# Performance work log

Hardware: AMD Instinct MI355X
Metric: run time of the kernel (lower is better)

Reference implementation:

```python
import jax, jax.numpy as jnp
import numpy as np

E, K, D_IN, D_OUT, D_HID = 16, 2, 1024, 1024, 2048

def setup_inputs() -> dict:
    key = jax.random.key(0)
    ks = jax.random.split(key, 6)
    s_in = 1.0 / np.sqrt(D_IN)
    s_hid = 1.0 / np.sqrt(D_HID)
    return {
        "x": jax.random.normal(ks[0], (4096, D_IN), dtype=jnp.float32),
        "gate_w": jax.random.uniform(ks[1], (E, D_IN), jnp.float32, -s_in, s_in),
        "w1": jax.random.uniform(ks[2], (E, D_HID, D_IN), jnp.float32, -s_in, s_in),
        "b1": jax.random.uniform(ks[3], (E, D_HID), jnp.float32, -s_in, s_in),
        "w2": jax.random.uniform(ks[4], (E, D_OUT, D_HID), jnp.float32, -s_hid, s_hid),
        "b2": jax.random.uniform(ks[5], (E, D_OUT), jnp.float32, -s_hid, s_hid),
    }

def reference(x, gate_w, w1, b1, w2, b2):
    # gate: [B, E]
    gate_scores = jnp.einsum('bi,ei->be', x, gate_w)
    topk_vals, topk_idxs = jax.lax.top_k(gate_scores, K)  # [B, K]
    topk_weights = jax.nn.softmax(topk_vals, axis=-1)     # [B, K]
    # dense all-expert MLP (faithful to reference): [B, E, D_OUT]
    h = jax.nn.relu(jnp.einsum('bi,ehi->beh', x, w1) + b1[None])
    expert_outputs = jnp.einsum('beh,eoh->beo', h, w2) + b2[None]
    # gather selected experts: [B, K, D_OUT]
    sel = jnp.take_along_axis(expert_outputs, topk_idxs[:, :, None], axis=1)
    return jnp.sum(sel * topk_weights[:, :, None], axis=1)
```

## Files before the change

kernel.cpp:

```cpp
#include <hip/hip_runtime.h>
#include <hip/hip_bf16.h>
#include <math.h>

#define B_TOK 4096
#define NE 16
#define DI 1024
#define DH 2048
#define DOUT 1024
#define NSLOT (B_TOK * 2)

typedef unsigned short u16;
typedef short bfrag __attribute__((ext_vector_type(8)));
typedef float f32x4 __attribute__((ext_vector_type(4)));
typedef u16 u16x8 __attribute__((ext_vector_type(8)));

__device__ __forceinline__ u16 f2bf(float f) {
    union { float f; unsigned u; } v; v.f = f;
    return (u16)((v.u + 0x7fffu + ((v.u >> 16) & 1u)) >> 16);
}

__device__ __forceinline__ void async16(const void* g, void* lds) {
    __builtin_amdgcn_global_load_lds(
        (const __attribute__((address_space(1))) void*)g,
        (__attribute__((address_space(3))) void*)lds,
        16, 0, 0);
}

__global__ void zero_init(float* __restrict__ out, int n4) {
    int i = blockIdx.x * blockDim.x + threadIdx.x;
    if (i < n4) ((float4*)out)[i] = make_float4(0.f, 0.f, 0.f, 0.f);
}

__global__ void convert_bf16(const float* __restrict__ src, u16* __restrict__ dst, int n8) {
    int i = blockIdx.x * blockDim.x + threadIdx.x;
    if (i >= n8) return;
    const float4* s4 = (const float4*)src;
    float4 a = s4[2 * i], b = s4[2 * i + 1];
    u16x8 r;
    r[0] = f2bf(a.x); r[1] = f2bf(a.y); r[2] = f2bf(a.z); r[3] = f2bf(a.w);
    r[4] = f2bf(b.x); r[5] = f2bf(b.y); r[6] = f2bf(b.z); r[7] = f2bf(b.w);
    ((u16x8*)dst)[i] = r;
}

__global__ __launch_bounds__(256) void gate_topk(
    const float* __restrict__ x, const float* __restrict__ gw,
    int* __restrict__ token_e, float* __restrict__ token_w)
{
    int wave = threadIdx.x >> 6, lane = threadIdx.x & 63;
    int t = blockIdx.x * 4 + wave;
    const float4* x4 = (const float4*)(x + (size_t)t * DI);
    const float4* g4 = (const float4*)gw;
    double acc[NE];
#pragma unroll
    for (int e = 0; e < NE; ++e) acc[e] = 0.0;
#pragma unroll
    for (int i = 0; i < 4; ++i) {
        float4 xv = x4[lane + i * 64];
#pragma unroll
        for (int e = 0; e < NE; ++e) {
            float4 gv = g4[e * 256 + lane + i * 64];
            acc[e] += (double)xv.x * gv.x + (double)xv.y * gv.y
                    + (double)xv.z * gv.z + (double)xv.w * gv.w;
        }
    }
#pragma unroll
    for (int e = 0; e < NE; ++e) {
        double v = acc[e];
        for (int off = 32; off; off >>= 1) v += __shfl_xor(v, off, 64);
        acc[e] = v;
    }
    if (lane == 0) {
        int e0 = 0; double v0 = acc[0];
#pragma unroll
        for (int e = 1; e < NE; ++e) if (acc[e] > v0) { v0 = acc[e]; e0 = e; }
        int e1 = -1; double v1 = -1e300;
#pragma unroll
        for (int e = 0; e < NE; ++e) if (e != e0 && acc[e] > v1) { v1 = acc[e]; e1 = e; }
        float d = expf((float)(v1 - v0));
        float w0 = 1.f / (1.f + d);
        float w1 = d * w0;
        token_e[2 * t] = e0; token_e[2 * t + 1] = e1;
        token_w[2 * t] = w0; token_w[2 * t + 1] = w1;
    }
}

__global__ __launch_bounds__(1024) void route(
    const int* __restrict__ token_e, const float* __restrict__ token_w,
    int* __restrict__ counts, int* __restrict__ offsets,
    int* __restrict__ slot_token, float* __restrict__ slot_wgt)
{
    __shared__ int lcnt[NE];
    __shared__ int lcur[NE];
    int tid = threadIdx.x;
    if (tid < NE) lcnt[tid] = 0;
    __syncthreads();
    for (int i = tid; i < NSLOT; i += 1024) atomicAdd(&lcnt[token_e[i]], 1);
    __syncthreads();
    if (tid == 0) {
        int s = 0;
        for (int e = 0; e < NE; ++e) {
            int c = lcnt[e];
            counts[e] = c; offsets[e] = s; lcur[e] = s; s += c;
        }
    }
    __syncthreads();
    for (int i = tid; i < NSLOT; i += 1024) {
        int e = token_e[i];
        int pos = atomicAdd(&lcur[e], 1);
        slot_token[pos] = i >> 1;
        slot_wgt[pos] = token_w[i];
    }
}

template <int PHASE>
__global__ __launch_bounds__(256) void moe_gemm(
    const u16* __restrict__ Abuf,
    const u16* __restrict__ Bbuf,
    const float* __restrict__ bias,
    const int* __restrict__ counts, const int* __restrict__ offsets,
    const int* __restrict__ slot_token, const float* __restrict__ slot_wgt,
    u16* __restrict__ hb, float* __restrict__ out)
{
    constexpr int KDIM = (PHASE == 1) ? DI : DH;
    constexpr int NDIM = (PHASE == 1) ? DH : DOUT;
    constexpr int NT = NDIM / 128;
    constexpr int MT = B_TOK / 128;
    constexpr int PER_XCD = (NE * NT * MT) / 8;

    const int id = blockIdx.x;
    const int wg = (id & 7) * PER_XCD + (id >> 3);
    const int e  = wg / (NT * MT);
    const int rem = wg % (NT * MT);
    const int nt = rem / MT;
    const int mt = rem % MT;

    const int cnt = counts[e];
    const int m0 = mt * 128;
    if (m0 >= cnt) return;
    const int n0 = nt * 128;
    const int sbase = offsets[e];

    __shared__ u16 ldsbuf[2][8192];

    const int tid = threadIdx.x;
    const int wv = tid >> 6, lane = tid & 63;
    const int lrow = lane >> 2, lkc = lane & 3;

    const int arow0 = wv * 16 + lrow;
    const int arow1 = 64 + wv * 16 + lrow;

    const u16* aptr0; const u16* aptr1;
    if (PHASE == 1) {
        int c = cnt - 1;
        int r0 = m0 + arow0; if (r0 > c) r0 = c;
        int r1 = m0 + arow1; if (r1 > c) r1 = c;
        aptr0 = Abuf + (size_t)slot_token[sbase + r0] * KDIM + lkc * 8;
        aptr1 = Abuf + (size_t)slot_token[sbase + r1] * KDIM + lkc * 8;
    } else {
        int s0 = sbase + m0 + arow0; if (s0 > NSLOT - 1) s0 = NSLOT - 1;
        int s1 = sbase + m0 + arow1; if (s1 > NSLOT - 1) s1 = NSLOT - 1;
        aptr0 = Abuf + (size_t)s0 * KDIM + lkc * 8;
        aptr1 = Abuf + (size_t)s1 * KDIM + lkc * 8;
    }
    const u16* bbase = Bbuf + (size_t)e * NDIM * KDIM;
    const u16* bptr0 = bbase + (size_t)(n0 + arow0) * KDIM + lkc * 8;
    const u16* bptr1 = bbase + (size_t)(n0 + arow1) * KDIM + lkc * 8;

    f32x4 acc[4][4];
#pragma unroll
    for (int i = 0; i < 4; ++i)
#pragma unroll
        for (int j = 0; j < 4; ++j) acc[i][j] = (f32x4){0.f, 0.f, 0.f, 0.f};

    const int wm = (wv & 1) * 64, wn = (wv >> 1) * 64;
    const int quad = lane >> 4, mr = lane & 15;
    const int aoff = (wm + mr) * 32 + quad * 8;
    const int boff = (wn + mr) * 32 + quad * 8;

    const int nk = KDIM / 32;

    {
        u16* base = &ldsbuf[0][0];
        async16(aptr0, base + wv * 512);
        async16(aptr1, base + 2048 + wv * 512);
        async16(bptr0, base + 4096 + wv * 512);
        async16(bptr1, base + 4096 + 2048 + wv * 512);
    }
    __syncthreads();

    for (int kt = 0; kt < nk; ++kt) {
        const int cur = kt & 1;
        if (kt + 1 < nk) {
            u16* base = &ldsbuf[cur ^ 1][0];
            const int ko = (kt + 1) * 32;
            async16(aptr0 + ko, base + wv * 512);
            async16(aptr1 + ko, base + 2048 + wv * 512);
            async16(bptr0 + ko, base + 4096 + wv * 512);
            async16(bptr1 + ko, base + 4096 + 2048 + wv * 512);
        }
        const u16* alds = &ldsbuf[cur][0];
        const u16* blds = alds + 4096;
        bfrag af[4], bf[4];
#pragma unroll
        for (int i = 0; i < 4; ++i) af[i] = *(const bfrag*)(alds + aoff + i * 512);
#pragma unroll
        for (int j = 0; j < 4; ++j) bf[j] = *(const bfrag*)(blds + boff + j * 512);
#pragma unroll
        for (int i = 0; i < 4; ++i)
#pragma unroll
            for (int j = 0; j < 4; ++j)
                acc[i][j] = __builtin_amdgcn_mfma_f32_16x16x32_bf16(af[i], bf[j], acc[i][j], 0, 0, 0);
        __syncthreads();
    }

    const float* bias_e = bias + e * NDIM;
    if constexpr (PHASE == 1) {
#pragma unroll
        for (int i = 0; i < 4; ++i) {
            int mbase = wm + i * 16 + quad * 4;
#pragma unroll
            for (int j = 0; j < 4; ++j) {
                int n = n0 + wn + j * 16 + mr;
                float bv = bias_e[n];
#pragma unroll
                for (int r = 0; r < 4; ++r) {
                    int m = m0 + mbase + r;
                    if (m < cnt) {
                        float v = acc[i][j][r] + bv;
                        v = v > 0.f ? v : 0.f;
                        hb[(size_t)(sbase + m) * DH + n] = f2bf(v);
                    }
                }
            }
        }
    } else {
#pragma unroll
        for (int i = 0; i < 4; ++i) {
            int mbase = wm + i * 16 + quad * 4;
#pragma unroll
            for (int r = 0; r < 4; ++r) {
                int m = m0 + mbase + r;
                if (m < cnt) {
                    int slot = sbase + m;
                    int tok = slot_token[slot];
                    float wgt = slot_wgt[slot];
                    float* orow = out + (size_t)tok * DOUT + n0 + wn;
#pragma unroll
                    for (int j = 0; j < 4; ++j) {
                        int nl = j * 16 + mr;
                        float v = wgt * (acc[i][j][r] + bias_e[n0 + wn + nl]);
                        atomicAdd(orow + nl, v);
                    }
                }
            }
        }
    }
}

extern "C" void kernel_launch(void* const* d_in, const int* in_sizes, int n_in,
                              void* d_out, int out_size, void* d_ws, size_t ws_size,
                              hipStream_t stream) {
    const float* x  = (const float*)d_in[0];
    const float* gw = (const float*)d_in[1];
    const float* w1 = (const float*)d_in[2];
    const float* b1 = (const float*)d_in[3];
    const float* w2 = (const float*)d_in[4];
    const float* b2 = (const float*)d_in[5];
    float* out = (float*)d_out;

    char* ws = (char*)d_ws;
    u16* xb = (u16*)ws;
    u16* wb = (u16*)(ws + 8388608);
    u16* hb = (u16*)(ws + 8388608 + 67108864);
    char* rb = ws + 109051904;
    int*   counts     = (int*)(rb);
    int*   offsets    = (int*)(rb + 64);
    int*   token_e    = (int*)(rb + 192);
    float* token_w    = (float*)(rb + 192 + 32768);
    int*   slot_token = (int*)(rb + 192 + 65536);
    float* slot_wgt   = (float*)(rb + 192 + 98304);

    zero_init<<<4096, 256, 0, stream>>>(out, (B_TOK * DOUT) / 4);
    convert_bf16<<<2048, 256, 0, stream>>>(x, xb, (B_TOK * DI) / 8);
    convert_bf16<<<16384, 256, 0, stream>>>(w1, wb, (NE * DH * DI) / 8);
    gate_topk<<<1024, 256, 0, stream>>>(x, gw, token_e, token_w);
    route<<<1, 1024, 0, stream>>>(token_e, token_w, counts, offsets, slot_token, slot_wgt);
    moe_gemm<1><<<NE * (DH / 128) * (B_TOK / 128), 256, 0, stream>>>(
        xb, wb, b1, counts, offsets, slot_token, slot_wgt, hb, out);
    convert_bf16<<<16384, 256, 0, stream>>>(w2, wb, (NE * DOUT * DH) / 8);
    moe_gemm<2><<<NE * (DOUT / 128) * (B_TOK / 128), 256, 0, stream>>>(
        hb, wb, b2, counts, offsets, slot_token, slot_wgt, hb, out);
}
```

Measured before the change: 500.7 us.

## Enlarge MoE GEMM tiles to 256-wide with 512 threads and swizzled LDS

Grows the grouped GEMM block tile from 128x128 to 256x256 (phase 1) or 256x128 (phase 2), with BK=64 and 8 waves per block, and adds an XOR swizzle on LDS columns to avoid bank conflicts on fragment reads. The aim is more reuse per LDS load and fewer global loads per MFMA. The cost is more LDS and registers per block, coarser padding waste on experts with ragged token counts (about 512 tokens per expert), and fewer blocks to spread across CUs.

Result: slower. 558.2 us (+11.5%).

```diff
diff --git a/kernel.cpp b/kernel.cpp
--- a/kernel.cpp
+++ b/kernel.cpp
@@ -113,7 +113,7 @@
 }
 
 template <int PHASE>
-__global__ __launch_bounds__(256) void moe_gemm(
+__global__ __launch_bounds__(512, 2) void moe_gemm(
     const u16* __restrict__ Abuf,
     const u16* __restrict__ Bbuf,
     const float* __restrict__ bias,
@@ -123,8 +123,18 @@
 {
     constexpr int KDIM = (PHASE == 1) ? DI : DH;
     constexpr int NDIM = (PHASE == 1) ? DH : DOUT;
-    constexpr int NT = NDIM / 128;
-    constexpr int MT = B_TOK / 128;
+    constexpr int BM = 256;
+    constexpr int BN = (PHASE == 1) ? 256 : 128;
+    constexpr int BK = 64;
+    constexpr int WTM = (PHASE == 1) ? 128 : 64;
+    constexpr int WTN = 64;
+    constexpr int MF = WTM / 16, NF = WTN / 16;
+    constexpr int GA = BM / 8;
+    constexpr int GB = BN / 8;
+    constexpr int GPW = (GA + GB) / 8;
+    constexpr int BUFU = (BM + BN) * BK;
+    constexpr int NT = NDIM / BN;
+    constexpr int MT = B_TOK / BM;
     constexpr int PER_XCD = (NE * NT * MT) / 8;
 
     const int id = blockIdx.x;
@@ -135,98 +145,94 @@
     const int mt = rem % MT;
 
     const int cnt = counts[e];
-    const int m0 = mt * 128;
+    const int m0 = mt * BM;
     if (m0 >= cnt) return;
-    const int n0 = nt * 128;
+    const int n0 = nt * BN;
     const int sbase = offsets[e];
 
-    __shared__ u16 ldsbuf[2][8192];
+    __shared__ u16 lds[2][BUFU];
 
     const int tid = threadIdx.x;
     const int wv = tid >> 6, lane = tid & 63;
-    const int lrow = lane >> 2, lkc = lane & 3;
-
-    const int arow0 = wv * 16 + lrow;
-    const int arow1 = 64 + wv * 16 + lrow;
-
-    const u16* aptr0; const u16* aptr1;
-    if (PHASE == 1) {
-        int c = cnt - 1;
-        int r0 = m0 + arow0; if (r0 > c) r0 = c;
-        int r1 = m0 + arow1; if (r1 > c) r1 = c;
-        aptr0 = Abuf + (size_t)slot_token[sbase + r0] * KDIM + lkc * 8;
-        aptr1 = Abuf + (size_t)slot_token[sbase + r1] * KDIM + lkc * 8;
-    } else {
-        int s0 = sbase + m0 + arow0; if (s0 > NSLOT - 1) s0 = NSLOT - 1;
-        int s1 = sbase + m0 + arow1; if (s1 > NSLOT - 1) s1 = NSLOT - 1;
-        aptr0 = Abuf + (size_t)s0 * KDIM + lkc * 8;
-        aptr1 = Abuf + (size_t)s1 * KDIM + lkc * 8;
-    }
-    const u16* bbase = Bbuf + (size_t)e * NDIM * KDIM;
-    const u16* bptr0 = bbase + (size_t)(n0 + arow0) * KDIM + lkc * 8;
-    const u16* bptr1 = bbase + (size_t)(n0 + arow1) * KDIM + lkc * 8;
-
-    f32x4 acc[4][4];
-#pragma unroll
-    for (int i = 0; i < 4; ++i)
-#pragma unroll
-        for (int j = 0; j < 4; ++j) acc[i][j] = (f32x4){0.f, 0.f, 0.f, 0.f};
-
-    const int wm = (wv & 1) * 64, wn = (wv >> 1) * 64;
     const int quad = lane >> 4, mr = lane & 15;
-    const int aoff = (wm + mr) * 32 + quad * 8;
-    const int boff = (wn + mr) * 32 + quad * 8;
-
-    const int nk = KDIM / 32;
-
-    {
-        u16* base = &ldsbuf[0][0];
-        async16(aptr0, base + wv * 512);
-        async16(aptr1, base + 2048 + wv * 512);
-        async16(bptr0, base + 4096 + wv * 512);
-        async16(bptr1, base + 4096 + 2048 + wv * 512);
-    }
+    const int wr = (PHASE == 1) ? (wv >> 2) : (wv >> 1);
+    const int wc = (PHASE == 1) ? (wv & 3)  : (wv & 1);
+
+    const int sr_ = lane >> 3, sc_ = lane & 7;
+    const int sw = (sc_ ^ sr_) * 8;
+    const u16* gptr[GPW];
+#pragma unroll
+    for (int j = 0; j < GPW; ++j) {
+        const int G = wv * GPW + j;
+        if (G < GA) {
+            int row = G * 8 + sr_;
+            if (PHASE == 1) {
+                int rr = m0 + row; if (rr > cnt - 1) rr = cnt - 1;
+                gptr[j] = Abuf + (size_t)slot_token[sbase + rr] * KDIM + sw;
+            } else {
+                int sr2 = sbase + m0 + row; if (sr2 > NSLOT - 1) sr2 = NSLOT - 1;
+                gptr[j] = Abuf + (size_t)sr2 * KDIM + sw;
+            }
+        } else {
+            int row = (G - GA) * 8 + sr_;
+            gptr[j] = Bbuf + (size_t)e * NDIM * KDIM + (size_t)(n0 + row) * KDIM + sw;
+        }
+    }
+
+    f32x4 acc[MF][NF];
+#pragma unroll
+    for (int i = 0; i < MF; ++i)
+#pragma unroll
+        for (int j = 0; j < NF; ++j) acc[i][j] = (f32x4){0.f, 0.f, 0.f, 0.f};
+
+    const int nk = KDIM / BK;
+
+#pragma unroll
+    for (int j = 0; j < GPW; ++j)
+        async16(gptr[j], &lds[0][(wv * GPW + j) * 512]);
     __syncthreads();
 
     for (int kt = 0; kt < nk; ++kt) {
-        const int cur = kt & 1;
+        const int bb = kt & 1;
         if (kt + 1 < nk) {
-            u16* base = &ldsbuf[cur ^ 1][0];
-            const int ko = (kt + 1) * 32;
-            async16(aptr0 + ko, base + wv * 512);
-            async16(aptr1 + ko, base + 2048 + wv * 512);
-            async16(bptr0 + ko, base + 4096 + wv * 512);
-            async16(bptr1 + ko, base + 4096 + 2048 + wv * 512);
-        }
-        const u16* alds = &ldsbuf[cur][0];
-        const u16* blds = alds + 4096;
-        bfrag af[4], bf[4];
-#pragma unroll
-        for (int i = 0; i < 4; ++i) af[i] = *(const bfrag*)(alds + aoff + i * 512);
-#pragma unroll
-        for (int j = 0; j < 4; ++j) bf[j] = *(const bfrag*)(blds + boff + j * 512);
-#pragma unroll
-        for (int i = 0; i < 4; ++i)
-#pragma unroll
-            for (int j = 0; j < 4; ++j)
-                acc[i][j] = __builtin_amdgcn_mfma_f32_16x16x32_bf16(af[i], bf[j], acc[i][j], 0, 0, 0);
+#pragma unroll
+            for (int j = 0; j < GPW; ++j)
+                async16(gptr[j] + (kt + 1) * BK, &lds[bb ^ 1][(wv * GPW + j) * 512]);
+        }
+        const u16* al = &lds[bb][0];
+        const u16* bl = al + BM * BK;
+#pragma unroll
+        for (int ks = 0; ks < 2; ++ks) {
+            const int cp = ((ks * 4 + quad) ^ (mr & 7)) * 8;
+            bfrag bf[NF];
+#pragma unroll
+            for (int nf = 0; nf < NF; ++nf)
+                bf[nf] = *(const bfrag*)(bl + (wc * WTN + nf * 16 + mr) * BK + cp);
+#pragma unroll
+            for (int mf = 0; mf < MF; ++mf) {
+                bfrag af = *(const bfrag*)(al + (wr * WTM + mf * 16 + mr) * BK + cp);
+#pragma unroll
+                for (int nf = 0; nf < NF; ++nf)
+                    acc[mf][nf] = __builtin_amdgcn_mfma_f32_16x16x32_bf16(af, bf[nf], acc[mf][nf], 0, 0, 0);
+            }
+        }
         __syncthreads();
     }
 
     const float* bias_e = bias + e * NDIM;
     if constexpr (PHASE == 1) {
 #pragma unroll
-        for (int i = 0; i < 4; ++i) {
-            int mbase = wm + i * 16 + quad * 4;
-#pragma unroll
-            for (int j = 0; j < 4; ++j) {
-                int n = n0 + wn + j * 16 + mr;
+        for (int mf = 0; mf < MF; ++mf) {
+            int mbase = wr * WTM + mf * 16 + quad * 4;
+#pragma unroll
+            for (int nf = 0; nf < NF; ++nf) {
+                int n = n0 + wc * WTN + nf * 16 + mr;
                 float bv = bias_e[n];
 #pragma unroll
                 for (int r = 0; r < 4; ++r) {
                     int m = m0 + mbase + r;
                     if (m < cnt) {
-                        float v = acc[i][j][r] + bv;
+                        float v = acc[mf][nf][r] + bv;
                         v = v > 0.f ? v : 0.f;
                         hb[(size_t)(sbase + m) * DH + n] = f2bf(v);
                     }
@@ -235,8 +241,8 @@
         }
     } else {
 #pragma unroll
-        for (int i = 0; i < 4; ++i) {
-            int mbase = wm + i * 16 + quad * 4;
+        for (int mf = 0; mf < MF; ++mf) {
+            int mbase = wr * WTM + mf * 16 + quad * 4;
 #pragma unroll
             for (int r = 0; r < 4; ++r) {
                 int m = m0 + mbase + r;
@@ -244,11 +250,11 @@
                     int slot = sbase + m;
                     int tok = slot_token[slot];
                     float wgt = slot_wgt[slot];
-                    float* orow = out + (size_t)tok * DOUT + n0 + wn;
-#pragma unroll
-                    for (int j = 0; j < 4; ++j) {
-                        int nl = j * 16 + mr;
-                        float v = wgt * (acc[i][j][r] + bias_e[n0 + wn + nl]);
+                    float* orow = out + (size_t)tok * DOUT + n0 + wc * WTN;
+#pragma unroll
+                    for (int nf = 0; nf < NF; ++nf) {
+                        int nl = nf * 16 + mr;
+                        float v = wgt * (acc[mf][nf][r] + bias_e[n0 + wc * WTN + nl]);
                         atomicAdd(orow + nl, v);
                     }
                 }
@@ -285,9 +291,9 @@
     convert_bf16<<<16384, 256, 0, stream>>>(w1, wb, (NE * DH * DI) / 8);
     gate_topk<<<1024, 256, 0, stream>>>(x, gw, token_e, token_w);
     route<<<1, 1024, 0, stream>>>(token_e, token_w, counts, offsets, slot_token, slot_wgt);
-    moe_gemm<1><<<NE * (DH / 128) * (B_TOK / 128), 256, 0, stream>>>(
+    moe_gemm<1><<<NE * (DH / 256) * (B_TOK / 256) * 16 / 16, 512, 0, stream>>>(
         xb, wb, b1, counts, offsets, slot_token, slot_wgt, hb, out);
     convert_bf16<<<16384, 256, 0, stream>>>(w2, wb, (NE * DOUT * DH) / 8);
-    moe_gemm<2><<<NE * (DOUT / 128) * (B_TOK / 128), 256, 0, stream>>>(
+    moe_gemm<2><<<NE * (DOUT / 128) * (B_TOK / 256), 512, 0, stream>>>(
         hb, wb, b2, counts, offsets, slot_token, slot_wgt, hb, out);
 }
```
